# Kernel optimization log

Hardware: AMD Instinct MI355X
Metric: run time of the kernel (lower is better)

The kernel has to match this reference:

```python
import jax, jax.numpy as jnp
import numpy as np

TOP_K = 2
TEMPERATURE = 2.0


def setup_inputs() -> dict:
    key = jax.random.key(0)
    k1, k2, k3 = jax.random.split(key, 3)
    x = jax.random.normal(k1, (16384, 2048), dtype=jnp.float32)
    gate_w = jax.random.normal(k2, (64, 2048), dtype=jnp.float32) * 0.02
    gate_b = jax.random.normal(k3, (64,), dtype=jnp.float32) * 0.02
    expert_maturity = jnp.ones((64,), dtype=jnp.int32)  # all mature -> top-k branch
    return {"x": x, "gate_w": gate_w, "gate_b": gate_b, "expert_maturity": expert_maturity}


def _routing(logits, expert_maturity):
    # branch 1: any immature expert -> temperature softmax over all experts
    def soft_branch(lg):
        return jax.nn.softmax(lg / TEMPERATURE, axis=-1)

    # branch 2: all mature -> top-k selection, softmax over selected, scatter into zeros
    def topk_branch(lg):
        top_w, top_idx = jax.lax.top_k(lg, TOP_K)          # [N, K]
        top_sm = jax.nn.softmax(top_w, axis=-1)            # [N, K]
        n = lg.shape[0]
        rows = jnp.arange(n)[:, None]                      # [N, 1]
        return jnp.zeros_like(lg).at[rows, top_idx].set(top_sm)

    any_immature = jnp.any(expert_maturity == 0)
    return jax.lax.cond(any_immature, soft_branch, topk_branch, logits)


def reference(x, gate_w, gate_b, expert_maturity):
    # logits = x @ W^T + b : [N, E]
    logits = jnp.einsum("nd,ed->ne", x, gate_w) + gate_b
    return _routing(logits, expert_maturity)
```

## Files before the change

### kernel.cpp

```cpp
#include <hip/hip_runtime.h>
#include <math.h>


#define NROWS 16384
#define DIM   2048
#define NEXP  64
#define BM    32
#define TPB   512
#define KSLICE 512
#define KSTEPS (KSLICE / 32)

typedef __attribute__((ext_vector_type(4))) float f32x4;
typedef __attribute__((ext_vector_type(8))) short bf16x8;

__global__ void wfrag_kernel(const float* __restrict__ gw,
                             unsigned short* __restrict__ wsH,
                             unsigned short* __restrict__ wsL) {
  int slot  = blockIdx.x * 256 + threadIdx.x;
  int lane  = slot & 63;
  int t     = (slot >> 6) & 3;
  int kstep = slot >> 8;
  int e  = 16 * t + (lane & 15);
  int k0 = kstep * 32 + (lane >> 4) * 8;
  const float* src = gw + (size_t)e * DIM + k0;
  bf16x8 vh, vl;
#pragma unroll
  for (int j = 0; j < 8; ++j) {
    float w = src[j];
    unsigned u = __float_as_uint(w);
    vh[j] = (short)(u >> 16);
    float hi = __uint_as_float(u & 0xffff0000u);
    float rl = w - hi;
    vl[j] = (short)(__float_as_uint(rl) >> 16);
  }
  ((bf16x8*)wsH)[slot] = vh;
  ((bf16x8*)wsL)[slot] = vl;
}

__global__ __launch_bounds__(TPB, 3)
void router_mfma(const float* __restrict__ x,
                 const unsigned short* __restrict__ wsH,
                 const unsigned short* __restrict__ wsL,
                 const float* __restrict__ gb,
                 const int* __restrict__ mat,
                 float* __restrict__ out) {
  __shared__ float slab[4 * BM * NEXP];
  __shared__ float p_a[BM], p_b[BM];
  __shared__ int   p_i[BM], p_j[BM];
  __shared__ int   s_flag;

  const int tid  = threadIdx.x;
  const int wave = tid >> 6;
  const int ksl  = wave >> 1;
  const int eh   = wave & 1;
  const int lane = tid & 63;
  const int m    = lane & 15;
  const int kg   = lane >> 4;
  const int row0 = blockIdx.x * BM;

  if (tid < 64) {
    unsigned long long b = __ballot(mat[lane] == 0);
    if (lane == 0) s_flag = (b != 0ull) ? 1 : 0;
  }

  f32x4 acc[2][2];
#pragma unroll
  for (int r = 0; r < 2; ++r)
#pragma unroll
    for (int t = 0; t < 2; ++t) acc[r][t] = (f32x4)0.0f;

  const size_t bbase = (size_t)(((ksl * KSTEPS) * 4 + 2 * eh) * 64 + lane);
  const bf16x8* bHp = (const bf16x8*)wsH + bbase;
  const bf16x8* bLp = (const bf16x8*)wsL + bbase;

  const float* xb = x + (size_t)(row0 + m) * DIM + ksl * KSLICE + kg * 8;

  float4 xr[2][2];
  xr[0][0] = *(const float4*)(xb);
  xr[0][1] = *(const float4*)(xb + 4);
  xr[1][0] = *(const float4*)(xb + 16 * DIM);
  xr[1][1] = *(const float4*)(xb + 16 * DIM + 4);
  bf16x8 bhc[2], blc[2];
#pragma unroll
  for (int t = 0; t < 2; ++t) {
    bhc[t] = bHp[t * 64];
    blc[t] = bLp[t * 64];
  }

#pragma unroll
  for (int s = 0; s < KSTEPS; ++s) {
    bf16x8 ah[2], al[2];
#pragma unroll
    for (int r = 0; r < 2; ++r) {
#pragma unroll
      for (int q = 0; q < 2; ++q) {
        float4 v = xr[r][q];
        float ff[4] = {v.x, v.y, v.z, v.w};
#pragma unroll
        for (int j = 0; j < 4; ++j) {
          unsigned u = __float_as_uint(ff[j]);
          ah[r][q * 4 + j] = (short)(u >> 16);
          float hi = __uint_as_float(u & 0xffff0000u);
          float rl = ff[j] - hi;
          al[r][q * 4 + j] = (short)(__float_as_uint(rl) >> 16);
        }
      }
    }
    const int sn = (s + 1 < KSTEPS) ? (s + 1) : s;
    {
      const float* xn = xb + sn * 32;
      xr[0][0] = *(const float4*)(xn);
      xr[0][1] = *(const float4*)(xn + 4);
      xr[1][0] = *(const float4*)(xn + 16 * DIM);
      xr[1][1] = *(const float4*)(xn + 16 * DIM + 4);
    }
    bf16x8 bhn[2], bln[2];
#pragma unroll
    for (int t = 0; t < 2; ++t) {
      bhn[t] = bHp[(size_t)sn * 256 + t * 64];
      bln[t] = bLp[(size_t)sn * 256 + t * 64];
    }
#pragma unroll
    for (int r = 0; r < 2; ++r) {
#pragma unroll
      for (int t = 0; t < 2; ++t) {
        acc[r][t] = __builtin_amdgcn_mfma_f32_16x16x32_bf16(ah[r], bhc[t], acc[r][t], 0, 0, 0);
        acc[r][t] = __builtin_amdgcn_mfma_f32_16x16x32_bf16(ah[r], blc[t], acc[r][t], 0, 0, 0);
        acc[r][t] = __builtin_amdgcn_mfma_f32_16x16x32_bf16(al[r], bhc[t], acc[r][t], 0, 0, 0);
      }
    }
#pragma unroll
    for (int t = 0; t < 2; ++t) { bhc[t] = bhn[t]; blc[t] = bln[t]; }
  }

  {
    float* sl = slab + ksl * (BM * NEXP);
#pragma unroll
    for (int r = 0; r < 2; ++r)
#pragma unroll
      for (int t = 0; t < 2; ++t)
#pragma unroll
        for (int reg = 0; reg < 4; ++reg)
          sl[(16 * r + kg * 4 + reg) * NEXP + 32 * eh + 16 * t + m] = acc[r][t][reg];
  }
  __syncthreads();

  for (int idx = tid; idx < BM * NEXP; idx += TPB) {
    float v = slab[idx] + slab[2048 + idx] + slab[4096 + idx] + slab[6144 + idx]
            + gb[idx & (NEXP - 1)];
    slab[idx] = v;
  }
  __syncthreads();

  const int flag = s_flag;

  if (tid < BM) {
    const float* rowp = slab + tid * NEXP;
    if (flag == 0) {
      float m1 = -1e30f, m2 = -1e30f;
      int i1 = 0, i2 = 0;
      for (int ee = 0; ee < NEXP; ++ee) {
        int e = (ee + tid) & (NEXP - 1);
        float v = rowp[e];
        if (v > m1) { m2 = m1; i2 = i1; m1 = v; i1 = e; }
        else if (v > m2) { m2 = v; i2 = e; }
      }
      float t = expf(m2 - m1);
      float pa = 1.0f / (1.0f + t);
      p_a[tid] = pa;
      p_b[tid] = t * pa;
      p_i[tid] = i1;
      p_j[tid] = i2;
    } else {
      float mx = -1e30f;
      for (int ee = 0; ee < NEXP; ++ee)
        mx = fmaxf(mx, rowp[(ee + tid) & (NEXP - 1)]);
      float ssum = 0.0f;
      for (int ee = 0; ee < NEXP; ++ee)
        ssum += expf((rowp[(ee + tid) & (NEXP - 1)] - mx) * 0.5f);
      p_a[tid] = mx;
      p_b[tid] = 1.0f / ssum;
    }
  }
  __syncthreads();

  {
    int q  = tid;
    int r  = q >> 4;
    int e0 = (q & 15) * 4;
    float4 v;
    if (flag == 0) {
      int i1 = p_i[r], i2 = p_j[r];
      float a = p_a[r], b = p_b[r];
      v.x = (e0 + 0 == i1) ? a : (e0 + 0 == i2) ? b : 0.0f;
      v.y = (e0 + 1 == i1) ? a : (e0 + 1 == i2) ? b : 0.0f;
      v.z = (e0 + 2 == i1) ? a : (e0 + 2 == i2) ? b : 0.0f;
      v.w = (e0 + 3 == i1) ? a : (e0 + 3 == i2) ? b : 0.0f;
    } else {
      float mx = p_a[r], inv = p_b[r];
      const float* rowp = slab + r * NEXP + e0;
      v.x = expf((rowp[0] - mx) * 0.5f) * inv;
      v.y = expf((rowp[1] - mx) * 0.5f) * inv;
      v.z = expf((rowp[2] - mx) * 0.5f) * inv;
      v.w = expf((rowp[3] - mx) * 0.5f) * inv;
    }
    *(float4*)(out + (size_t)(row0 + r) * NEXP + e0) = v;
  }
}

extern "C" void kernel_launch(void* const* d_in, const int* in_sizes, int n_in,
                              void* d_out, int out_size, void* d_ws, size_t ws_size,
                              hipStream_t stream) {
  const float* x  = (const float*)d_in[0];
  const float* gw = (const float*)d_in[1];
  const float* gb = (const float*)d_in[2];
  const int*   mt = (const int*)d_in[3];
  float* outp = (float*)d_out;
  (void)in_sizes; (void)n_in; (void)out_size; (void)ws_size;

  unsigned short* wsH = (unsigned short*)d_ws;
  unsigned short* wsL = wsH + 64 * DIM;

  wfrag_kernel<<<64, 256, 0, stream>>>(gw, wsH, wsL);
  router_mfma<<<NROWS / BM, TPB, 0, stream>>>(x, wsH, wsL, gb, mt, outp);
}
```

Before: 218.7 us.

## Shrink row tile to 16 with 4-wave blocks and 4-deep x prefetch

Cuts the block tile from 32 rows and 8 waves to 16 rows and 4 waves. Each wave now covers all 64 experts for one 16-row group over its K-slice, instead of splitting experts across two waves. The x loads become a 4-step-ahead register ring buffer in place of single-step prefetch, and the weight fragments are loaded each step without prefetch. The aim is more blocks and occupancy plus deeper latency hiding for the streamed x, at the cost of reading the weight fragments twice as often per row and losing reuse of B across two row groups.

```diff
diff --git a/kernel.cpp b/kernel.cpp
--- a/kernel.cpp
+++ b/kernel.cpp
@@ -5,8 +5,8 @@
 #define NROWS 16384
 #define DIM   2048
 #define NEXP  64
-#define BM    32
-#define TPB   512
+#define BM    16
+#define TPB   256
 #define KSLICE 512
 #define KSTEPS (KSLICE / 32)
 
@@ -37,7 +37,7 @@
   ((bf16x8*)wsL)[slot] = vl;
 }
 
-__global__ __launch_bounds__(TPB, 3)
+__global__ __launch_bounds__(TPB, 4)
 void router_mfma(const float* __restrict__ x,
                  const unsigned short* __restrict__ wsH,
                  const unsigned short* __restrict__ wsL,
@@ -50,9 +50,7 @@
   __shared__ int   s_flag;
 
   const int tid  = threadIdx.x;
-  const int wave = tid >> 6;
-  const int ksl  = wave >> 1;
-  const int eh   = wave & 1;
+  const int ksl  = tid >> 6;
   const int lane = tid & 63;
   const int m    = lane & 15;
   const int kg   = lane >> 4;
@@ -63,90 +61,71 @@
     if (lane == 0) s_flag = (b != 0ull) ? 1 : 0;
   }
 
-  f32x4 acc[2][2];
-#pragma unroll
-  for (int r = 0; r < 2; ++r)
-#pragma unroll
-    for (int t = 0; t < 2; ++t) acc[r][t] = (f32x4)0.0f;
-
-  const size_t bbase = (size_t)(((ksl * KSTEPS) * 4 + 2 * eh) * 64 + lane);
+  f32x4 acc[4];
+#pragma unroll
+  for (int t = 0; t < 4; ++t) acc[t] = (f32x4)0.0f;
+
+  const size_t bbase = (size_t)((ksl * KSTEPS * 4) * 64 + lane);
   const bf16x8* bHp = (const bf16x8*)wsH + bbase;
   const bf16x8* bLp = (const bf16x8*)wsL + bbase;
 
   const float* xb = x + (size_t)(row0 + m) * DIM + ksl * KSLICE + kg * 8;
 
-  float4 xr[2][2];
-  xr[0][0] = *(const float4*)(xb);
-  xr[0][1] = *(const float4*)(xb + 4);
-  xr[1][0] = *(const float4*)(xb + 16 * DIM);
-  xr[1][1] = *(const float4*)(xb + 16 * DIM + 4);
-  bf16x8 bhc[2], blc[2];
-#pragma unroll
-  for (int t = 0; t < 2; ++t) {
-    bhc[t] = bHp[t * 64];
-    blc[t] = bLp[t * 64];
-  }
-
-#pragma unroll
+  float4 xr[4][2];
+#pragma unroll
+  for (int p = 0; p < 4; ++p) {
+    xr[p][0] = *(const float4*)(xb + p * 32);
+    xr[p][1] = *(const float4*)(xb + p * 32 + 4);
+  }
+
+#pragma unroll 4
   for (int s = 0; s < KSTEPS; ++s) {
-    bf16x8 ah[2], al[2];
-#pragma unroll
-    for (int r = 0; r < 2; ++r) {
-#pragma unroll
-      for (int q = 0; q < 2; ++q) {
-        float4 v = xr[r][q];
-        float ff[4] = {v.x, v.y, v.z, v.w};
-#pragma unroll
-        for (int j = 0; j < 4; ++j) {
-          unsigned u = __float_as_uint(ff[j]);
-          ah[r][q * 4 + j] = (short)(u >> 16);
-          float hi = __uint_as_float(u & 0xffff0000u);
-          float rl = ff[j] - hi;
-          al[r][q * 4 + j] = (short)(__float_as_uint(rl) >> 16);
-        }
+    const int slot = s & 3;
+    bf16x8 ah, al;
+#pragma unroll
+    for (int q = 0; q < 2; ++q) {
+      float4 v = xr[slot][q];
+      float ff[4] = {v.x, v.y, v.z, v.w};
+#pragma unroll
+      for (int j = 0; j < 4; ++j) {
+        unsigned u = __float_as_uint(ff[j]);
+        ah[q * 4 + j] = (short)(u >> 16);
+        float hi = __uint_as_float(u & 0xffff0000u);
+        float rl = ff[j] - hi;
+        al[q * 4 + j] = (short)(__float_as_uint(rl) >> 16);
       }
     }
-    const int sn = (s + 1 < KSTEPS) ? (s + 1) : s;
     {
-      const float* xn = xb + sn * 32;
-      xr[0][0] = *(const float4*)(xn);
-      xr[0][1] = *(const float4*)(xn + 4);
-      xr[1][0] = *(const float4*)(xn + 16 * DIM);
-      xr[1][1] = *(const float4*)(xn + 16 * DIM + 4);
-    }
-    bf16x8 bhn[2], bln[2];
-#pragma unroll
-    for (int t = 0; t < 2; ++t) {
-      bhn[t] = bHp[(size_t)sn * 256 + t * 64];
-      bln[t] = bLp[(size_t)sn * 256 + t * 64];
-    }
-#pragma unroll
-    for (int r = 0; r < 2; ++r) {
-#pragma unroll
-      for (int t = 0; t < 2; ++t) {
-        acc[r][t] = __builtin_amdgcn_mfma_f32_16x16x32_bf16(ah[r], bhc[t], acc[r][t], 0, 0, 0);
-        acc[r][t] = __builtin_amdgcn_mfma_f32_16x16x32_bf16(ah[r], blc[t], acc[r][t], 0, 0, 0);
-        acc[r][t] = __builtin_amdgcn_mfma_f32_16x16x32_bf16(al[r], bhc[t], acc[r][t], 0, 0, 0);
-      }
-    }
-#pragma unroll
-    for (int t = 0; t < 2; ++t) { bhc[t] = bhn[t]; blc[t] = bln[t]; }
+      const int sp = (s + 4 < KSTEPS) ? (s + 4) : s;
+      xr[slot][0] = *(const float4*)(xb + sp * 32);
+      xr[slot][1] = *(const float4*)(xb + sp * 32 + 4);
+    }
+    bf16x8 bh[4], bl[4];
+#pragma unroll
+    for (int t = 0; t < 4; ++t) {
+      bh[t] = bHp[(size_t)s * 256 + t * 64];
+      bl[t] = bLp[(size_t)s * 256 + t * 64];
+    }
+#pragma unroll
+    for (int t = 0; t < 4; ++t) {
+      acc[t] = __builtin_amdgcn_mfma_f32_16x16x32_bf16(ah, bh[t], acc[t], 0, 0, 0);
+      acc[t] = __builtin_amdgcn_mfma_f32_16x16x32_bf16(ah, bl[t], acc[t], 0, 0, 0);
+      acc[t] = __builtin_amdgcn_mfma_f32_16x16x32_bf16(al, bh[t], acc[t], 0, 0, 0);
+    }
   }
 
   {
     float* sl = slab + ksl * (BM * NEXP);
 #pragma unroll
-    for (int r = 0; r < 2; ++r)
-#pragma unroll
-      for (int t = 0; t < 2; ++t)
-#pragma unroll
-        for (int reg = 0; reg < 4; ++reg)
-          sl[(16 * r + kg * 4 + reg) * NEXP + 32 * eh + 16 * t + m] = acc[r][t][reg];
+    for (int t = 0; t < 4; ++t)
+#pragma unroll
+      for (int reg = 0; reg < 4; ++reg)
+        sl[(kg * 4 + reg) * NEXP + 16 * t + m] = acc[t][reg];
   }
   __syncthreads();
 
   for (int idx = tid; idx < BM * NEXP; idx += TPB) {
-    float v = slab[idx] + slab[2048 + idx] + slab[4096 + idx] + slab[6144 + idx]
+    float v = slab[idx] + slab[1024 + idx] + slab[2048 + idx] + slab[3072 + idx]
             + gb[idx & (NEXP - 1)];
     slab[idx] = v;
   }
```

Result: no change. 221.6 us (+1.3%).
